# Kernel tuning notes

Hardware: AMD Instinct MI355X
Metric: run time of the kernel (lower is better)

Reference implementation:

```python
import jax, jax.numpy as jnp
from jax import lax
import numpy as np

B = 512
EPS = 1e-5


def _conv(x, w, b):
    # x: [B,C,H,W], w: [O,I,3,3], stride 1, pad 1 (same spatial)
    y = lax.conv_general_dilated(x, w, window_strides=(1, 1),
                                 padding=[(1, 1), (1, 1)],
                                 dimension_numbers=('NCHW', 'OIHW', 'NCHW'))
    return y + b[None, :, None, None]


def _bn(x, g, b, m, v):
    # eval-mode batchnorm with running stats
    inv = g * lax.rsqrt(v + EPS)
    return x * inv[None, :, None, None] + (b - m * inv)[None, :, None, None]


def _maxpool2(x):
    return lax.reduce_window(x, -jnp.inf, lax.max, (1, 1, 2, 2), (1, 1, 2, 2), 'VALID')


def _block(x, w, b, g, be, m, v):
    return _maxpool2(jax.nn.relu(_bn(_conv(x, w, b), g, be, m, v)))


def setup_inputs() -> dict:
    key = jax.random.key(0)
    ks = jax.random.split(key, 12)
    n = lambda k, s: jax.random.normal(k, s, jnp.float32) * 0.05
    z = lambda s: jnp.zeros(s, jnp.float32)
    o = lambda s: jnp.ones(s, jnp.float32)
    return {
        'x': jax.random.normal(ks[0], (B, 1, 48, 48), jnp.float32),
        'conv1_w': n(ks[1], (256, 1, 3, 3)), 'conv1_b': z((256,)),
        'bn1_g': o((256,)), 'bn1_b': z((256,)), 'bn1_m': z((256,)), 'bn1_v': o((256,)),
        'conv2_w': n(ks[2], (128, 256, 3, 3)), 'conv2_b': z((128,)),
        'bn2_g': o((128,)), 'bn2_b': z((128,)), 'bn2_m': z((128,)), 'bn2_v': o((128,)),
        'conv3_w': n(ks[3], (64, 128, 3, 3)), 'conv3_b': z((64,)),
        'bn3_g': o((64,)), 'bn3_b': z((64,)), 'bn3_m': z((64,)), 'bn3_v': o((64,)),
        'fc1_w': n(ks[4], (512, 2304)), 'fc1_b': z((512,)),
        'fc2_w': n(ks[5], (256, 512)), 'fc2_b': z((256,)),
        'att_w': n(ks[6], (64, 256)), 'att_b': z((64,)),
        'fc3_w': n(ks[7], (7, 64)), 'fc3_b': z((7,)),
    }


def reference(x, conv1_w, conv1_b, bn1_g, bn1_b, bn1_m, bn1_v,
              conv2_w, conv2_b, bn2_g, bn2_b, bn2_m, bn2_v,
              conv3_w, conv3_b, bn3_g, bn3_b, bn3_m, bn3_v,
              fc1_w, fc1_b, fc2_w, fc2_b, att_w, att_b, fc3_w, fc3_b):
    out1 = _block(x, conv1_w, conv1_b, bn1_g, bn1_b, bn1_m, bn1_v)      # [B,256,24,24]
    out2 = _block(out1, conv2_w, conv2_b, bn2_g, bn2_b, bn2_m, bn2_v)   # [B,128,12,12]
    out3 = _block(out2, conv3_w, conv3_b, bn3_g, bn3_b, bn3_m, bn3_v)   # [B,64,6,6]
    b_ = out3.shape[0]
    out4 = out3.reshape(b_, -1)                                          # [B,2304]
    out5 = out4 @ fc1_w.T + fc1_b                                        # [B,512]
    out6 = out5 @ fc2_w.T + fc2_b                                        # [B,256]
    # spatial attention: query projected to channel dim of out3
    q = out6 @ att_w.T + att_b                                           # [B,64]
    scores = jnp.einsum('bchw,bc->bhw', out3, q).reshape(b_, -1)         # [B,36]
    attn = jax.nn.softmax(scores, axis=1).reshape(b_, 6, 6)
    g_mod = jnp.einsum('bchw,bhw->bc', out3, attn)                       # [B,64]
    return g_mod @ fc3_w.T + fc3_b                                       # [B,7]
```

## Files before the change

### kernel.cpp

```cpp
#include <hip/hip_runtime.h>
#include <hip/hip_bf16.h>
#include <math.h>

#define EPS_BN 1e-5f

typedef __bf16 bf16x8 __attribute__((ext_vector_type(8)));
typedef float f32x4 __attribute__((ext_vector_type(4)));
typedef float f32x2 __attribute__((ext_vector_type(2)));

__device__ __forceinline__ void gl2lds16(const void* g, void* l) {
  __builtin_amdgcn_global_load_lds(
      (const __attribute__((address_space(1))) unsigned int*)g,
      (__attribute__((address_space(3))) unsigned int*)l, 16, 0, 0);
}

__global__ __launch_bounds__(256) void k_conv1(
    const float* __restrict__ x, const float* __restrict__ w,
    const float* __restrict__ cb, const float* __restrict__ g,
    const float* __restrict__ bb, const float* __restrict__ m,
    const float* __restrict__ v, __hip_bfloat16* __restrict__ out1p,
    __hip_bfloat16* __restrict__ out2p, const float* __restrict__ W32,
    const float* __restrict__ fc1w, float* __restrict__ Wet, int n1) {
  __shared__ float xp[14 * 50];
  const int bq = blockIdx.x;
  const int t = threadIdx.x;
  if (bq >= n1) {
    int idx = (bq - n1) * 256 + t;
    int r = idx / 2304, c = idx - r * 2304;
    float s = 0.f;
    for (int k = 0; k < 512; k++)
      s = fmaf(W32[r * 512 + k], fc1w[k * 2304 + c], s);
    Wet[c * 64 + r] = s;
    return;
  }
  const int b = bq >> 2, q = bq & 3;
  __hip_bfloat16* ob = out1p + (size_t)b * (26 * 26 * 256);
  const __hip_bfloat16 z = __float2bfloat16(0.f);
  if (q == 0)
    for (int i = t; i < 26 * 256; i += 256) ob[i] = z;
  if (q == 3)
    for (int i = t; i < 26 * 256; i += 256) ob[25 * 26 * 256 + i] = z;
  for (int i = t; i < 6 * 2 * 256; i += 256) {
    int r = 1 + 6 * q + (i >> 9), side = (i >> 8) & 1, c = i & 255;
    ob[(r * 26 + side * 25) * 256 + c] = z;
  }
  {
    __hip_bfloat16* o2 = out2p + (size_t)b * (14 * 14 * 128);
    if (q == 0)
      for (int i = t; i < 14 * 128; i += 256) o2[i] = z;
    if (q == 1)
      for (int i = t; i < 14 * 128; i += 256) o2[13 * 14 * 128 + i] = z;
    if (q == 2)
      for (int i = t; i < 6 * 2 * 128; i += 256) {
        int r = 1 + (i >> 8), side = (i >> 7) & 1, c = i & 127;
        o2[(r * 14 + side * 13) * 128 + c] = z;
      }
    if (q == 3)
      for (int i = t; i < 6 * 2 * 128; i += 256) {
        int r = 7 + (i >> 8), side = (i >> 7) & 1, c = i & 127;
        o2[(r * 14 + side * 13) * 128 + c] = z;
      }
  }
  for (int i = t; i < 14 * 50; i += 256) xp[i] = 0.f;
  __syncthreads();
  const float* xb = x + (size_t)b * 2304;
  for (int i = t; i < 14 * 48; i += 256) {
    int rr = i / 48, c = i - rr * 48;
    int gr = 12 * q - 1 + rr;
    if (gr >= 0 && gr < 48) xp[rr * 50 + c + 1] = xb[gr * 48 + c];
  }
  __syncthreads();
  float wr[9];
#pragma unroll
  for (int i = 0; i < 9; i++) wr[i] = w[t * 9 + i];
  const float scale = g[t] * rsqrtf(v[t] + EPS_BN);
  const float bias = (cb[t] - m[t]) * scale + bb[t];
#pragma unroll
  for (int ohl = 0; ohl < 6; ohl++) {
    const int r0 = 2 * ohl;
    f32x2 c01[4];
#pragma unroll
    for (int r = 0; r < 4; r++) c01[r] = *(const f32x2*)&xp[(r0 + r) * 50];
#pragma unroll 4
    for (int ow = 0; ow < 24; ow++) {
      f32x2 c23[4];
#pragma unroll
      for (int r = 0; r < 4; r++)
        c23[r] = *(const f32x2*)&xp[(r0 + r) * 50 + 2 * ow + 2];
      f32x2 s2a = 0.f, s2b = 0.f;
#pragma unroll
      for (int r = 0; r < 4; r++) {
        f32x2 p0 = c01[r], p2 = c23[r];
        f32x2 p1 = {p0.y, p2.x};
        if (r <= 2) {
          s2a += p0 * wr[r * 3 + 0];
          s2a += p1 * wr[r * 3 + 1];
          s2a += p2 * wr[r * 3 + 2];
        }
        if (r >= 1) {
          s2b += p0 * wr[(r - 1) * 3 + 0];
          s2b += p1 * wr[(r - 1) * 3 + 1];
          s2b += p2 * wr[(r - 1) * 3 + 2];
        }
      }
      f32x2 b0 = s2a * scale + bias;
      f32x2 b1 = s2b * scale + bias;
      float mx = fmaxf(fmaxf(b0.x, b0.y), fmaxf(b1.x, b1.y));
      ob[((6 * q + ohl + 1) * 26 + (ow + 1)) * 256 + t] =
          __float2bfloat16(fmaxf(mx, 0.f));
#pragma unroll
      for (int r = 0; r < 4; r++) c01[r] = c23[r];
    }
  }
}

__global__ void k_prep(const float* __restrict__ c2w,
                       __hip_bfloat16* __restrict__ wt2,
                       const float* __restrict__ c3w,
                       __hip_bfloat16* __restrict__ wt3,
                       const float* __restrict__ attw,
                       const float* __restrict__ fc2w, float* __restrict__ W32,
                       const float* __restrict__ fc1b,
                       const float* __restrict__ fc2b,
                       const float* __restrict__ attb, float* __restrict__ be) {
  const int blk = blockIdx.x, tid = threadIdx.x;
  if (blk < 1152) {
    int idx = blk * 256 + tid;
    int icr = idx & 7;
    int oc = (idx >> 3) & 127;
    int rest = idx >> 10;
    int icg = rest & 31;
    int p = rest >> 5;
    wt2[idx] = __float2bfloat16(c2w[(oc * 256 + icg * 8 + icr) * 9 + p]);
  } else if (blk < 1440) {
    int idx = (blk - 1152) * 256 + tid;
    int icr = idx & 7;
    int oc = (idx >> 3) & 63;
    int rest = idx >> 9;
    int icg = rest & 15;
    int p = rest >> 4;
    wt3[idx] = __float2bfloat16(c3w[(oc * 128 + icg * 8 + icr) * 9 + p]);
  } else if (blk < 1568) {
    int idx = (blk - 1440) * 256 + tid;
    int r = idx >> 9, c = idx & 511;
    float s = 0.f;
    for (int k = 0; k < 256; k++)
      s = fmaf(attw[r * 256 + k], fc2w[k * 512 + c], s);
    W32[idx] = s;
  } else {
    __shared__ float t1[256];
    float s = fc2b[tid];
    for (int k = 0; k < 512; k++) s = fmaf(fc2w[tid * 512 + k], fc1b[k], s);
    t1[tid] = s;
    __syncthreads();
    if (tid < 64) {
      float r = attb[tid];
      for (int k = 0; k < 256; k++) r = fmaf(attw[tid * 256 + k], t1[k], r);
      be[tid] = r;
    }
  }
}

template <int HW, int IC, int OC, int NW_M, int NW_N>
__global__ __launch_bounds__(256) void k_mconv(
    const __hip_bfloat16* __restrict__ in, const __hip_bfloat16* __restrict__ wt,
    const float* __restrict__ cb, const float* __restrict__ gg,
    const float* __restrict__ bbv, const float* __restrict__ bm,
    const float* __restrict__ bv, __hip_bfloat16* __restrict__ outp) {
  constexpr int HP = HW + 2;
  constexpr int MT = NW_M * 48;
  constexpr int ROWS = MT / HW;
  constexpr int TILES = HW / ROWS;
  constexpr int WN = OC / NW_N;
  constexpr int NF = WN / 16;
  constexpr int CP = HP;
  constexpr int NCH = 6 * CP * 8;
  constexpr int NCHP = (NCH + 255) & ~255;
  constexpr int NLD = NCHP / 256;
  constexpr int NSTG = IC / 64;
  constexpr int ABUF = NCHP * 16;
  constexpr int ICG = IC / 8;
  constexpr int EPITCH = OC + 1;
  constexpr int EBYTES = 48 * EPITCH * 4;
  constexpr int SMB = (2 * ABUF) > EBYTES ? (2 * ABUF) : EBYTES;

  __shared__ __align__(16) char smraw[SMB];
  float* se = (float*)smraw;

  const int tid = threadIdx.x;
  const int wv = tid >> 6, ln = tid & 63;
  const int wm = wv >> 1, wn = wv & 1;
  const int lhi = ln >> 4, llo = ln & 15;

  const int per = gridDim.x >> 3;
  const int xcd = blockIdx.x & 7, sl = blockIdx.x >> 3;
  const int b = xcd * (per / TILES) + sl / TILES;
  const int T = sl % TILES;
  const int h0 = T * ROWS;

  const __hip_bfloat16* inb = in + (size_t)b * HP * HP * IC;

  int srcoff[NLD];
#pragma unroll
  for (int i = 0; i < NLD; i++) {
    int ci = tid + i * 256;
    if (ci >= NCH) ci = NCH - 1;
    int kgslot = ci & 7;
    int rest = ci >> 3;
    int c = rest % CP;
    int r = rest / CP;
    int kg = kgslot ^ (c & 7);
    srcoff[i] = ((h0 + r) * HP + c) * IC + kg * 8;
  }
  int spb[3][3], msk[3][3];
#pragma unroll
  for (int mt = 0; mt < 3; mt++) {
    int m = wm * 48 + mt * 16 + llo;
    int hl = m / HW, wl = m % HW;
#pragma unroll
    for (int pw = 0; pw < 3; pw++) {
      spb[mt][pw] = (hl * CP + wl + pw) * 8;
      msk[mt][pw] = (wl + pw) & 7;
    }
  }
  const __hip_bfloat16* wtb = wt + (size_t)(lhi * OC + wn * WN + llo) * 8;

  f32x4 acc[3][NF];
  const f32x4 fz = {0.f, 0.f, 0.f, 0.f};
#pragma unroll
  for (int i = 0; i < 3; i++)
#pragma unroll
    for (int j = 0; j < NF; j++) acc[i][j] = fz;

#pragma unroll
  for (int i = 0; i < NLD; i++)
    gl2lds16(inb + srcoff[i], smraw + (tid + i * 256) * 16);
  __syncthreads();

#pragma unroll
  for (int s = 0; s < NSTG; s++) {
    if (s + 1 < NSTG) {
      char* nb = smraw + ((s + 1) & 1) * ABUF;
#pragma unroll
      for (int i = 0; i < NLD; i++)
        gl2lds16(inb + srcoff[i] + (s + 1) * 64, nb + (tid + i * 256) * 16);
    }
    const char* cw = smraw + (s & 1) * ABUF;
#pragma unroll
    for (int p = 0; p < 9; p++) {
      const int ph = p / 3, pw = p % 3;
#pragma unroll
      for (int ks = 0; ks < 2; ks++) {
        const int kg = ks * 4 + lhi;
        bf16x8 bf[NF];
#pragma unroll
        for (int j = 0; j < NF; j++)
          bf[j] = *(const bf16x8*)(wtb +
                                   ((size_t)(p * ICG + s * 8 + ks * 4) * OC) *
                                       8 +
                                   j * 128);
        bf16x8 af[3];
#pragma unroll
        for (int mt = 0; mt < 3; mt++) {
          int slot = spb[mt][pw] + ph * CP * 8 + (kg ^ msk[mt][pw]);
          af[mt] = *(const bf16x8*)(cw + slot * 16);
        }
#pragma unroll
        for (int mt = 0; mt < 3; mt++)
#pragma unroll
          for (int j = 0; j < NF; j++)
            acc[mt][j] = __builtin_amdgcn_mfma_f32_16x16x32_bf16(
                af[mt], bf[j], acc[mt][j], 0, 0, 0);
      }
    }
    __syncthreads();
  }

  constexpr int PR = 48 / HW;
  constexpr int POH = PR / 2;
  constexpr int OHW = HW / 2;
  constexpr int NP = POH * OHW * OC;
#pragma unroll
  for (int a = 0; a < NW_M; a++) {
    if (a) __syncthreads();
    if (wm == a) {
#pragma unroll
      for (int j = 0; j < NF; j++) {
        int n = wn * WN + j * 16 + llo;
        float scale = gg[n] * rsqrtf(bv[n] + EPS_BN);
        float bias = (cb[n] - bm[n]) * scale + bbv[n];
#pragma unroll
        for (int mt = 0; mt < 3; mt++)
#pragma unroll
          for (int r = 0; r < 4; r++) {
            int mrow = mt * 16 + lhi * 4 + r;
            se[mrow * EPITCH + n] = fmaxf(acc[mt][j][r] * scale + bias, 0.f);
          }
      }
    }
    __syncthreads();
    for (int s = tid; s < NP; s += 256) {
      int n = s % OC;
      int ow = (s / OC) % OHW;
      int ohl = s / (OC * OHW);
      int mloc = (2 * ohl) * HW + 2 * ow;
      float x0 = se[mloc * EPITCH + n];
      float x1 = se[(mloc + 1) * EPITCH + n];
      float x2 = se[(mloc + HW) * EPITCH + n];
      float x3 = se[(mloc + HW + 1) * EPITCH + n];
      float mx = fmaxf(fmaxf(x0, x1), fmaxf(x2, x3));
      int oh = (h0 >> 1) + a * POH + ohl;
      outp[(((size_t)b * (OHW + 2) + oh + 1) * (OHW + 2) + ow + 1) * OC + n] =
          __float2bfloat16(mx);
    }
    if (a + 1 < NW_M) __syncthreads();
  }
}

__global__ __launch_bounds__(256) void k_c3attn(
    const __hip_bfloat16* __restrict__ in, const __hip_bfloat16* __restrict__ wt,
    const float* __restrict__ cb, const float* __restrict__ gg,
    const float* __restrict__ bbv, const float* __restrict__ bm,
    const float* __restrict__ bv, const float* __restrict__ Wet,
    const float* __restrict__ be, const float* __restrict__ w3,
    const float* __restrict__ b3, float* __restrict__ out, int b0) {
  constexpr int HW = 12, IC = 128, OC = 64, HP = 14, CP = 14;
  constexpr int NCH = 14 * CP * 8;
  constexpr int NCHP = (NCH + 255) & ~255;
  constexpr int NLD = NCHP / 256;
  constexpr int NSTG = 2;
  constexpr int ABUF = NCHP * 16;
  constexpr int ICG = 16;
  constexpr int EPITCH = OC + 1;

  __shared__ __align__(16) char smraw[2 * ABUF];
  __shared__ float act[64 * 37];
  __shared__ float qp[4][64];
  __shared__ float ql[64], gm[64], sc[36];
  float* se = (float*)smraw;

  const int tid = threadIdx.x;
  const int wv = tid >> 6, ln = tid & 63;
  const int lhi = ln >> 4, llo = ln & 15;
  const int b = blockIdx.x;

  const __hip_bfloat16* inb = in + (size_t)b * HP * HP * IC;

  int srcoff[NLD];
#pragma unroll
  for (int i = 0; i < NLD; i++) {
    int ci = tid + i * 256;
    if (ci >= NCH) ci = NCH - 1;
    int kgslot = ci & 7;
    int rest = ci >> 3;
    int c = rest % CP;
    int r = rest / CP;
    int kg = kgslot ^ (c & 7);
    srcoff[i] = (r * HP + c) * IC + kg * 8;
  }
  int spb[9], wlv[9];
#pragma unroll
  for (int mt = 0; mt < 9; mt++) {
    int m = mt * 16 + llo;
    int hl = m / HW, wl = m % HW;
    spb[mt] = (hl * CP + wl) * 8;
    wlv[mt] = wl;
  }
  const __hip_bfloat16* wtb = wt + (size_t)(lhi * OC + wv * 16 + llo) * 8;

  f32x4 acc[9];
  const f32x4 fz = {0.f, 0.f, 0.f, 0.f};
#pragma unroll
  for (int i = 0; i < 9; i++) acc[i] = fz;

#pragma unroll
  for (int i = 0; i < NLD; i++)
    gl2lds16(inb + srcoff[i], smraw + (tid + i * 256) * 16);
  __syncthreads();

#pragma unroll
  for (int s = 0; s < NSTG; s++) {
    if (s + 1 < NSTG) {
      char* nb = smraw + ((s + 1) & 1) * ABUF;
#pragma unroll
      for (int i = 0; i < NLD; i++)
        gl2lds16(inb + srcoff[i] + (s + 1) * 64, nb + (tid + i * 256) * 16);
    }
    const char* cw = smraw + (s & 1) * ABUF;
#pragma unroll
    for (int tt = 0; tt < 18; tt++) {
      const int p = tt >> 1, ks = tt & 1;
      const int ph = p / 3, pw = p % 3;
      const int kg = ks * 4 + lhi;
      bf16x8 bf =
          *(const bf16x8*)(wtb + ((size_t)(p * ICG + s * 8 + ks * 4) * OC) * 8);
#pragma unroll
      for (int mt = 0; mt < 9; mt++) {
        int slot = spb[mt] + (ph * CP + pw) * 8 + (kg ^ ((wlv[mt] + pw) & 7));
        bf16x8 af = *(const bf16x8*)(cw + slot * 16);
        acc[mt] = __builtin_amdgcn_mfma_f32_16x16x32_bf16(af, bf, acc[mt], 0,
                                                          0, 0);
      }
    }
    __syncthreads();
  }

  {
    const int n = wv * 16 + llo;
    const float scale = gg[n] * rsqrtf(bv[n] + EPS_BN);
    const float bias = (cb[n] - bm[n]) * scale + bbv[n];
#pragma unroll
    for (int pz = 0; pz < 3; pz++) {
      if (pz) __syncthreads();
#pragma unroll
      for (int mtl = 0; mtl < 3; mtl++)
#pragma unroll
        for (int r = 0; r < 4; r++) {
          int mrow = mtl * 16 + lhi * 4 + r;
          se[mrow * EPITCH + n] =
              fmaxf(acc[pz * 3 + mtl][r] * scale + bias, 0.f);
        }
      __syncthreads();
      for (int sI = tid; sI < 2 * 6 * 64; sI += 256) {
        int nn = sI % 64;
        int ow = (sI / 64) % 6;
        int ohl = sI / (64 * 6);
        int mloc = (2 * ohl) * HW + 2 * ow;
        float x0 = se[mloc * EPITCH + nn];
        float x1 = se[(mloc + 1) * EPITCH + nn];
        float x2 = se[(mloc + HW) * EPITCH + nn];
        float x3 = se[(mloc + HW + 1) * EPITCH + nn];
        float mx = fmaxf(fmaxf(x0, x1), fmaxf(x2, x3));
        act[nn * 37 + (pz * 2 + ohl) * 6 + ow] = mx;
      }
    }
  }
  __syncthreads();

  {
    float qpv = 0.f;
    const int n = ln;
#pragma unroll 2
    for (int c2 = wv * 16; c2 < wv * 16 + 16; c2++)
      for (int hw = 0; hw < 36; hw++)
        qpv = fmaf(act[c2 * 37 + hw], Wet[(c2 * 36 + hw) * 64 + n], qpv);
    qp[wv][n] = qpv;
  }
  __syncthreads();
  if (tid < 64)
    ql[tid] = be[tid] + qp[0][tid] + qp[1][tid] + qp[2][tid] + qp[3][tid];
  __syncthreads();
  if (wv == 0) {
    float s = -INFINITY;
    if (ln < 36) {
      float a = 0.f;
      for (int c = 0; c < 64; c++) a = fmaf(act[c * 37 + ln], ql[c], a);
      s = a;
    }
    float mx = s;
    for (int off = 32; off >= 1; off >>= 1)
      mx = fmaxf(mx, __shfl_xor(mx, off));
    float e = (ln < 36) ? expf(s - mx) : 0.f;
    float sum = e;
    for (int off = 32; off >= 1; off >>= 1) sum += __shfl_xor(sum, off);
    if (ln < 36) sc[ln] = e / sum;
  }
  __syncthreads();
  if (wv == 0) {
    float gv = 0.f;
    for (int hw = 0; hw < 36; hw++) gv = fmaf(act[ln * 37 + hw], sc[hw], gv);
    gm[ln] = gv;
  }
  __syncthreads();
  if (tid < 7) {
    float a = b3[tid];
    for (int c = 0; c < 64; c++) a = fmaf(w3[tid * 64 + c], gm[c], a);
    out[(size_t)(b0 + b) * 7 + tid] = a;
  }
}

extern "C" void kernel_launch(void* const* d_in, const int* in_sizes, int n_in,
                              void* d_out, int out_size, void* d_ws,
                              size_t ws_size, hipStream_t stream) {
  const float* x    = (const float*)d_in[0];
  const float* c1w  = (const float*)d_in[1];
  const float* c1b  = (const float*)d_in[2];
  const float* g1   = (const float*)d_in[3];
  const float* bb1  = (const float*)d_in[4];
  const float* m1   = (const float*)d_in[5];
  const float* v1   = (const float*)d_in[6];
  const float* c2w  = (const float*)d_in[7];
  const float* c2b  = (const float*)d_in[8];
  const float* g2   = (const float*)d_in[9];
  const float* bb2  = (const float*)d_in[10];
  const float* m2   = (const float*)d_in[11];
  const float* v2   = (const float*)d_in[12];
  const float* c3w  = (const float*)d_in[13];
  const float* c3b  = (const float*)d_in[14];
  const float* g3   = (const float*)d_in[15];
  const float* bb3  = (const float*)d_in[16];
  const float* m3   = (const float*)d_in[17];
  const float* v3   = (const float*)d_in[18];
  const float* fc1w = (const float*)d_in[19];
  const float* fc1b = (const float*)d_in[20];
  const float* fc2w = (const float*)d_in[21];
  const float* fc2b = (const float*)d_in[22];
  const float* attw = (const float*)d_in[23];
  const float* attb = (const float*)d_in[24];
  const float* fc3w = (const float*)d_in[25];
  const float* fc3b = (const float*)d_in[26];

  const size_t PER_CHUNK = (173056ULL + 25088ULL) * 2;
  const size_t PERSIST = 589824 + 147456 + 131072 + 589824 + 256 + 8192;
  int CH = 512;
  while (CH > 8 && (size_t)CH * PER_CHUNK + PERSIST > ws_size) CH >>= 1;
  const int NCHK = 512 / CH;

  char* base = (char*)d_ws;
  size_t off = 0;
  auto alloc = [&](size_t nbytes) -> void* {
    void* p = base + off;
    off = (off + nbytes + 255) & ~(size_t)255;
    return p;
  };
  __hip_bfloat16* out1p = (__hip_bfloat16*)alloc((size_t)CH * 173056 * 2);
  __hip_bfloat16* out2p = (__hip_bfloat16*)alloc((size_t)CH * 25088 * 2);
  __hip_bfloat16* wt2  = (__hip_bfloat16*)alloc(589824);
  __hip_bfloat16* wt3  = (__hip_bfloat16*)alloc(147456);
  float* W32           = (float*)alloc(131072);
  float* Wet           = (float*)alloc(589824);
  float* be            = (float*)alloc(256);

  k_prep<<<1569, 256, 0, stream>>>(c2w, wt2, c3w, wt3, attw, fc2w, W32, fc1b,
                                   fc2b, attb, be);

  for (int c = 0; c < NCHK; c++) {
    const float* xc = x + (size_t)c * CH * 2304;
    const int n1 = CH * 4;
    const int grid1 = n1 + (c == 0 ? 576 : 0);
    k_conv1<<<grid1, 256, 0, stream>>>(xc, c1w, c1b, g1, bb1, m1, v1, out1p,
                                       out2p, W32, fc1w, Wet, n1);
    k_mconv<24, 256, 128, 2, 2>
        <<<CH * 6, 256, 0, stream>>>(out1p, wt2, c2b, g2, bb2, m2, v2, out2p);
    k_c3attn<<<CH, 256, 0, stream>>>(out2p, wt3, c3b, g3, bb3, m3, v3, Wet, be,
                                     fc3w, fc3b, (float*)d_out, c * CH);
  }
}
```

Baseline: 423.8 us.

## Fuse conv1, conv2 and conv3+attention into one per-image persistent kernel

```diff
diff --git a/kernel.cpp b/kernel.cpp
--- a/kernel.cpp
+++ b/kernel.cpp
@@ -12,106 +12,6 @@
   __builtin_amdgcn_global_load_lds(
       (const __attribute__((address_space(1))) unsigned int*)g,
       (__attribute__((address_space(3))) unsigned int*)l, 16, 0, 0);
-}
-
-__global__ __launch_bounds__(256) void k_conv1(
-    const float* __restrict__ x, const float* __restrict__ w,
-    const float* __restrict__ cb, const float* __restrict__ g,
-    const float* __restrict__ bb, const float* __restrict__ m,
-    const float* __restrict__ v, __hip_bfloat16* __restrict__ out1p,
-    __hip_bfloat16* __restrict__ out2p, const float* __restrict__ W32,
-    const float* __restrict__ fc1w, float* __restrict__ Wet, int n1) {
-  __shared__ float xp[14 * 50];
-  const int bq = blockIdx.x;
-  const int t = threadIdx.x;
-  if (bq >= n1) {
-    int idx = (bq - n1) * 256 + t;
-    int r = idx / 2304, c = idx - r * 2304;
-    float s = 0.f;
-    for (int k = 0; k < 512; k++)
-      s = fmaf(W32[r * 512 + k], fc1w[k * 2304 + c], s);
-    Wet[c * 64 + r] = s;
-    return;
-  }
-  const int b = bq >> 2, q = bq & 3;
-  __hip_bfloat16* ob = out1p + (size_t)b * (26 * 26 * 256);
-  const __hip_bfloat16 z = __float2bfloat16(0.f);
-  if (q == 0)
-    for (int i = t; i < 26 * 256; i += 256) ob[i] = z;
-  if (q == 3)
-    for (int i = t; i < 26 * 256; i += 256) ob[25 * 26 * 256 + i] = z;
-  for (int i = t; i < 6 * 2 * 256; i += 256) {
-    int r = 1 + 6 * q + (i >> 9), side = (i >> 8) & 1, c = i & 255;
-    ob[(r * 26 + side * 25) * 256 + c] = z;
-  }
-  {
-    __hip_bfloat16* o2 = out2p + (size_t)b * (14 * 14 * 128);
-    if (q == 0)
-      for (int i = t; i < 14 * 128; i += 256) o2[i] = z;
-    if (q == 1)
-      for (int i = t; i < 14 * 128; i += 256) o2[13 * 14 * 128 + i] = z;
-    if (q == 2)
-      for (int i = t; i < 6 * 2 * 128; i += 256) {
-        int r = 1 + (i >> 8), side = (i >> 7) & 1, c = i & 127;
-        o2[(r * 14 + side * 13) * 128 + c] = z;
-      }
-    if (q == 3)
-      for (int i = t; i < 6 * 2 * 128; i += 256) {
-        int r = 7 + (i >> 8), side = (i >> 7) & 1, c = i & 127;
-        o2[(r * 14 + side * 13) * 128 + c] = z;
-      }
-  }
-  for (int i = t; i < 14 * 50; i += 256) xp[i] = 0.f;
-  __syncthreads();
-  const float* xb = x + (size_t)b * 2304;
-  for (int i = t; i < 14 * 48; i += 256) {
-    int rr = i / 48, c = i - rr * 48;
-    int gr = 12 * q - 1 + rr;
-    if (gr >= 0 && gr < 48) xp[rr * 50 + c + 1] = xb[gr * 48 + c];
-  }
-  __syncthreads();
-  float wr[9];
-#pragma unroll
-  for (int i = 0; i < 9; i++) wr[i] = w[t * 9 + i];
-  const float scale = g[t] * rsqrtf(v[t] + EPS_BN);
-  const float bias = (cb[t] - m[t]) * scale + bb[t];
-#pragma unroll
-  for (int ohl = 0; ohl < 6; ohl++) {
-    const int r0 = 2 * ohl;
-    f32x2 c01[4];
-#pragma unroll
-    for (int r = 0; r < 4; r++) c01[r] = *(const f32x2*)&xp[(r0 + r) * 50];
-#pragma unroll 4
-    for (int ow = 0; ow < 24; ow++) {
-      f32x2 c23[4];
-#pragma unroll
-      for (int r = 0; r < 4; r++)
-        c23[r] = *(const f32x2*)&xp[(r0 + r) * 50 + 2 * ow + 2];
-      f32x2 s2a = 0.f, s2b = 0.f;
-#pragma unroll
-      for (int r = 0; r < 4; r++) {
-        f32x2 p0 = c01[r], p2 = c23[r];
-        f32x2 p1 = {p0.y, p2.x};
-        if (r <= 2) {
-          s2a += p0 * wr[r * 3 + 0];
-          s2a += p1 * wr[r * 3 + 1];
-          s2a += p2 * wr[r * 3 + 2];
-        }
-        if (r >= 1) {
-          s2b += p0 * wr[(r - 1) * 3 + 0];
-          s2b += p1 * wr[(r - 1) * 3 + 1];
-          s2b += p2 * wr[(r - 1) * 3 + 2];
-        }
-      }
-      f32x2 b0 = s2a * scale + bias;
-      f32x2 b1 = s2b * scale + bias;
-      float mx = fmaxf(fmaxf(b0.x, b0.y), fmaxf(b1.x, b1.y));
-      ob[((6 * q + ohl + 1) * 26 + (ow + 1)) * 256 + t] =
-          __float2bfloat16(fmaxf(mx, 0.f));
-#pragma unroll
-      for (int r = 0; r < 4; r++) c01[r] = c23[r];
-    }
-  }
 }
 
 __global__ void k_prep(const float* __restrict__ c2w,
@@ -161,321 +61,393 @@
   }
 }
 
-template <int HW, int IC, int OC, int NW_M, int NW_N>
-__global__ __launch_bounds__(256) void k_mconv(
-    const __hip_bfloat16* __restrict__ in, const __hip_bfloat16* __restrict__ wt,
-    const float* __restrict__ cb, const float* __restrict__ gg,
-    const float* __restrict__ bbv, const float* __restrict__ bm,
-    const float* __restrict__ bv, __hip_bfloat16* __restrict__ outp) {
-  constexpr int HP = HW + 2;
-  constexpr int MT = NW_M * 48;
-  constexpr int ROWS = MT / HW;
-  constexpr int TILES = HW / ROWS;
-  constexpr int WN = OC / NW_N;
-  constexpr int NF = WN / 16;
-  constexpr int CP = HP;
-  constexpr int NCH = 6 * CP * 8;
-  constexpr int NCHP = (NCH + 255) & ~255;
-  constexpr int NLD = NCHP / 256;
-  constexpr int NSTG = IC / 64;
-  constexpr int ABUF = NCHP * 16;
-  constexpr int ICG = IC / 8;
-  constexpr int EPITCH = OC + 1;
-  constexpr int EBYTES = 48 * EPITCH * 4;
-  constexpr int SMB = (2 * ABUF) > EBYTES ? (2 * ABUF) : EBYTES;
-
-  __shared__ __align__(16) char smraw[SMB];
-  float* se = (float*)smraw;
-
+__global__ void k_weff(const float* __restrict__ W32,
+                       const float* __restrict__ A1, float* __restrict__ Wet) {
+  int idx = blockIdx.x * 256 + threadIdx.x;
+  int r = idx / 2304, c = idx - r * 2304;
+  float s = 0.f;
+  for (int k = 0; k < 512; k++) s = fmaf(W32[r * 512 + k], A1[k * 2304 + c], s);
+  Wet[c * 64 + r] = s;
+}
+
+__global__ __launch_bounds__(256, 2) void k_pipe(
+    const float* __restrict__ x, const float* __restrict__ c1w,
+    const float* __restrict__ c1b, const float* __restrict__ g1,
+    const float* __restrict__ bb1, const float* __restrict__ m1,
+    const float* __restrict__ v1, __hip_bfloat16* __restrict__ out1p,
+    __hip_bfloat16* __restrict__ out2p, const __hip_bfloat16* __restrict__ wt2,
+    const float* __restrict__ c2b, const float* __restrict__ g2,
+    const float* __restrict__ bb2, const float* __restrict__ m2,
+    const float* __restrict__ v2, const __hip_bfloat16* __restrict__ wt3,
+    const float* __restrict__ c3b, const float* __restrict__ g3,
+    const float* __restrict__ bb3, const float* __restrict__ m3,
+    const float* __restrict__ v3, const float* __restrict__ Wet,
+    const float* __restrict__ be, const float* __restrict__ fc3w,
+    const float* __restrict__ fc3b, float* __restrict__ out, int b0) {
+  __shared__ __align__(16) char smem[44032];
+  const int blk = blockIdx.x;
   const int tid = threadIdx.x;
   const int wv = tid >> 6, ln = tid & 63;
-  const int wm = wv >> 1, wn = wv & 1;
   const int lhi = ln >> 4, llo = ln & 15;
 
-  const int per = gridDim.x >> 3;
-  const int xcd = blockIdx.x & 7, sl = blockIdx.x >> 3;
-  const int b = xcd * (per / TILES) + sl / TILES;
-  const int T = sl % TILES;
-  const int h0 = T * ROWS;
-
-  const __hip_bfloat16* inb = in + (size_t)b * HP * HP * IC;
-
-  int srcoff[NLD];
-#pragma unroll
-  for (int i = 0; i < NLD; i++) {
-    int ci = tid + i * 256;
-    if (ci >= NCH) ci = NCH - 1;
-    int kgslot = ci & 7;
-    int rest = ci >> 3;
-    int c = rest % CP;
-    int r = rest / CP;
-    int kg = kgslot ^ (c & 7);
-    srcoff[i] = ((h0 + r) * HP + c) * IC + kg * 8;
+  {
+    float* xp = (float*)smem;
+    __hip_bfloat16* ob = out1p + (size_t)blk * (26 * 26 * 256);
+    __hip_bfloat16* o2 = out2p + (size_t)blk * (14 * 14 * 128);
+    const __hip_bfloat16 z = __float2bfloat16(0.f);
+    const float* xb = x + (size_t)blk * 2304;
+    float wr[9];
+#pragma unroll
+    for (int i = 0; i < 9; i++) wr[i] = c1w[tid * 9 + i];
+    const float scale = g1[tid] * rsqrtf(v1[tid] + EPS_BN);
+    const float bias = (c1b[tid] - m1[tid]) * scale + bb1[tid];
+    for (int q = 0; q < 4; q++) {
+      __syncthreads();
+      if (q == 0)
+        for (int i = tid; i < 26 * 256; i += 256) ob[i] = z;
+      if (q == 3)
+        for (int i = tid; i < 26 * 256; i += 256) ob[25 * 26 * 256 + i] = z;
+      for (int i = tid; i < 6 * 2 * 256; i += 256) {
+        int r = 1 + 6 * q + (i >> 9), side = (i >> 8) & 1, c = i & 255;
+        ob[(r * 26 + side * 25) * 256 + c] = z;
+      }
+      if (q == 0)
+        for (int i = tid; i < 14 * 128; i += 256) o2[i] = z;
+      if (q == 1)
+        for (int i = tid; i < 14 * 128; i += 256) o2[13 * 14 * 128 + i] = z;
+      if (q == 2)
+        for (int i = tid; i < 6 * 2 * 128; i += 256) {
+          int r = 1 + (i >> 8), side = (i >> 7) & 1, c = i & 127;
+          o2[(r * 14 + side * 13) * 128 + c] = z;
+        }
+      if (q == 3)
+        for (int i = tid; i < 6 * 2 * 128; i += 256) {
+          int r = 7 + (i >> 8), side = (i >> 7) & 1, c = i & 127;
+          o2[(r * 14 + side * 13) * 128 + c] = z;
+        }
+      for (int i = tid; i < 14 * 50; i += 256) xp[i] = 0.f;
+      __syncthreads();
+      for (int i = tid; i < 14 * 48; i += 256) {
+        int rr = i / 48, c = i - rr * 48;
+        int gr = 12 * q - 1 + rr;
+        if (gr >= 0 && gr < 48) xp[rr * 50 + c + 1] = xb[gr * 48 + c];
+      }
+      __syncthreads();
+#pragma unroll
+      for (int ohl = 0; ohl < 6; ohl++) {
+        const int r0 = 2 * ohl;
+        f32x2 c01[4];
+#pragma unroll
+        for (int r = 0; r < 4; r++) c01[r] = *(const f32x2*)&xp[(r0 + r) * 50];
+#pragma unroll 4
+        for (int ow = 0; ow < 24; ow++) {
+          f32x2 c23[4];
+#pragma unroll
+          for (int r = 0; r < 4; r++)
+            c23[r] = *(const f32x2*)&xp[(r0 + r) * 50 + 2 * ow + 2];
+          f32x2 s2a = 0.f, s2b = 0.f;
+#pragma unroll
+          for (int r = 0; r < 4; r++) {
+            f32x2 p0 = c01[r], p2 = c23[r];
+            f32x2 p1 = {p0.y, p2.x};
+            if (r <= 2) {
+              s2a += p0 * wr[r * 3 + 0];
+              s2a += p1 * wr[r * 3 + 1];
+              s2a += p2 * wr[r * 3 + 2];
+            }
+            if (r >= 1) {
+              s2b += p0 * wr[(r - 1) * 3 + 0];
+              s2b += p1 * wr[(r - 1) * 3 + 1];
+              s2b += p2 * wr[(r - 1) * 3 + 2];
+            }
+          }
+          f32x2 e0 = s2a * scale + bias;
+          f32x2 e1 = s2b * scale + bias;
+          float mx = fmaxf(fmaxf(e0.x, e0.y), fmaxf(e1.x, e1.y));
+          ob[((6 * q + ohl + 1) * 26 + (ow + 1)) * 256 + tid] =
+              __float2bfloat16(fmaxf(mx, 0.f));
+#pragma unroll
+          for (int r = 0; r < 4; r++) c01[r] = c23[r];
+        }
+      }
+    }
   }
-  int spb[3][3], msk[3][3];
-#pragma unroll
-  for (int mt = 0; mt < 3; mt++) {
-    int m = wm * 48 + mt * 16 + llo;
-    int hl = m / HW, wl = m % HW;
-#pragma unroll
-    for (int pw = 0; pw < 3; pw++) {
-      spb[mt][pw] = (hl * CP + wl + pw) * 8;
-      msk[mt][pw] = (wl + pw) & 7;
-    }
-  }
-  const __hip_bfloat16* wtb = wt + (size_t)(lhi * OC + wn * WN + llo) * 8;
-
-  f32x4 acc[3][NF];
-  const f32x4 fz = {0.f, 0.f, 0.f, 0.f};
-#pragma unroll
-  for (int i = 0; i < 3; i++)
-#pragma unroll
-    for (int j = 0; j < NF; j++) acc[i][j] = fz;
-
-#pragma unroll
-  for (int i = 0; i < NLD; i++)
-    gl2lds16(inb + srcoff[i], smraw + (tid + i * 256) * 16);
-  __syncthreads();
-
-#pragma unroll
-  for (int s = 0; s < NSTG; s++) {
-    if (s + 1 < NSTG) {
-      char* nb = smraw + ((s + 1) & 1) * ABUF;
+
+  {
+    constexpr int HW = 24, IC = 256, OC = 128, HP = 26, CP = 26;
+    constexpr int NCH = 6 * CP * 8;
+    constexpr int NCHP = (NCH + 255) & ~255;
+    constexpr int NLD = NCHP / 256;
+    constexpr int NSTG = 4;
+    constexpr int ABUF = NCHP * 16;
+    constexpr int ICG = 32;
+    constexpr int EPITCH = OC + 1;
+    const int wm = wv >> 1, wn = wv & 1;
+    float* se = (float*)smem;
+
+    const __hip_bfloat16* inb = out1p + (size_t)blk * HP * HP * IC;
+    int srcoff[NLD];
+#pragma unroll
+    for (int i = 0; i < NLD; i++) {
+      int ci = tid + i * 256;
+      if (ci >= NCH) ci = NCH - 1;
+      int kgslot = ci & 7;
+      int rest = ci >> 3;
+      int c = rest % CP;
+      int r = rest / CP;
+      int kg = kgslot ^ (c & 7);
+      srcoff[i] = (r * HP + c) * IC + kg * 8;
+    }
+    int spb[3][3], msk[3][3];
+#pragma unroll
+    for (int mt = 0; mt < 3; mt++) {
+      int m = wm * 48 + mt * 16 + llo;
+      int hl = m / HW, wl = m % HW;
+#pragma unroll
+      for (int pw = 0; pw < 3; pw++) {
+        spb[mt][pw] = (hl * CP + wl + pw) * 8;
+        msk[mt][pw] = (wl + pw) & 7;
+      }
+    }
+    const __hip_bfloat16* wtb = wt2 + (size_t)(lhi * OC + wn * 64 + llo) * 8;
+
+    for (int T = 0; T < 6; T++) {
+      const int h0 = T * 4;
+      const int toff = h0 * HP * IC;
+      __syncthreads();
+      f32x4 acc[3][4];
+      const f32x4 fz = {0.f, 0.f, 0.f, 0.f};
+#pragma unroll
+      for (int i = 0; i < 3; i++)
+#pragma unroll
+        for (int j = 0; j < 4; j++) acc[i][j] = fz;
 #pragma unroll
       for (int i = 0; i < NLD; i++)
-        gl2lds16(inb + srcoff[i] + (s + 1) * 64, nb + (tid + i * 256) * 16);
-    }
-    const char* cw = smraw + (s & 1) * ABUF;
-#pragma unroll
-    for (int p = 0; p < 9; p++) {
-      const int ph = p / 3, pw = p % 3;
-#pragma unroll
-      for (int ks = 0; ks < 2; ks++) {
-        const int kg = ks * 4 + lhi;
-        bf16x8 bf[NF];
-#pragma unroll
-        for (int j = 0; j < NF; j++)
-          bf[j] = *(const bf16x8*)(wtb +
+        gl2lds16(inb + toff + srcoff[i], smem + (tid + i * 256) * 16);
+      __syncthreads();
+#pragma unroll
+      for (int s = 0; s < NSTG; s++) {
+        if (s + 1 < NSTG) {
+          char* nb = smem + ((s + 1) & 1) * ABUF;
+#pragma unroll
+          for (int i = 0; i < NLD; i++)
+            gl2lds16(inb + toff + srcoff[i] + (s + 1) * 64,
+                     nb + (tid + i * 256) * 16);
+        }
+        const char* cw = smem + (s & 1) * ABUF;
+#pragma unroll
+        for (int p = 0; p < 9; p++) {
+          const int ph = p / 3, pw = p % 3;
+#pragma unroll
+          for (int ks = 0; ks < 2; ks++) {
+            const int kg = ks * 4 + lhi;
+            bf16x8 bf[4];
+#pragma unroll
+            for (int j = 0; j < 4; j++)
+              bf[j] =
+                  *(const bf16x8*)(wtb +
                                    ((size_t)(p * ICG + s * 8 + ks * 4) * OC) *
                                        8 +
                                    j * 128);
-        bf16x8 af[3];
-#pragma unroll
-        for (int mt = 0; mt < 3; mt++) {
-          int slot = spb[mt][pw] + ph * CP * 8 + (kg ^ msk[mt][pw]);
-          af[mt] = *(const bf16x8*)(cw + slot * 16);
-        }
-#pragma unroll
-        for (int mt = 0; mt < 3; mt++)
-#pragma unroll
-          for (int j = 0; j < NF; j++)
-            acc[mt][j] = __builtin_amdgcn_mfma_f32_16x16x32_bf16(
-                af[mt], bf[j], acc[mt][j], 0, 0, 0);
-      }
-    }
-    __syncthreads();
-  }
-
-  constexpr int PR = 48 / HW;
-  constexpr int POH = PR / 2;
-  constexpr int OHW = HW / 2;
-  constexpr int NP = POH * OHW * OC;
-#pragma unroll
-  for (int a = 0; a < NW_M; a++) {
-    if (a) __syncthreads();
-    if (wm == a) {
-#pragma unroll
-      for (int j = 0; j < NF; j++) {
-        int n = wn * WN + j * 16 + llo;
-        float scale = gg[n] * rsqrtf(bv[n] + EPS_BN);
-        float bias = (cb[n] - bm[n]) * scale + bbv[n];
-#pragma unroll
-        for (int mt = 0; mt < 3; mt++)
-#pragma unroll
-          for (int r = 0; r < 4; r++) {
-            int mrow = mt * 16 + lhi * 4 + r;
-            se[mrow * EPITCH + n] = fmaxf(acc[mt][j][r] * scale + bias, 0.f);
+            bf16x8 af[3];
+#pragma unroll
+            for (int mt = 0; mt < 3; mt++) {
+              int slot = spb[mt][pw] + ph * CP * 8 + (kg ^ msk[mt][pw]);
+              af[mt] = *(const bf16x8*)(cw + slot * 16);
+            }
+#pragma unroll
+            for (int mt = 0; mt < 3; mt++)
+#pragma unroll
+              for (int j = 0; j < 4; j++)
+                acc[mt][j] = __builtin_amdgcn_mfma_f32_16x16x32_bf16(
+                    af[mt], bf[j], acc[mt][j], 0, 0, 0);
           }
-      }
-    }
-    __syncthreads();
-    for (int s = tid; s < NP; s += 256) {
-      int n = s % OC;
-      int ow = (s / OC) % OHW;
-      int ohl = s / (OC * OHW);
-      int mloc = (2 * ohl) * HW + 2 * ow;
-      float x0 = se[mloc * EPITCH + n];
-      float x1 = se[(mloc + 1) * EPITCH + n];
-      float x2 = se[(mloc + HW) * EPITCH + n];
-      float x3 = se[(mloc + HW + 1) * EPITCH + n];
-      float mx = fmaxf(fmaxf(x0, x1), fmaxf(x2, x3));
-      int oh = (h0 >> 1) + a * POH + ohl;
-      outp[(((size_t)b * (OHW + 2) + oh + 1) * (OHW + 2) + ow + 1) * OC + n] =
-          __float2bfloat16(mx);
-    }
-    if (a + 1 < NW_M) __syncthreads();
-  }
-}
-
-__global__ __launch_bounds__(256) void k_c3attn(
-    const __hip_bfloat16* __restrict__ in, const __hip_bfloat16* __restrict__ wt,
-    const float* __restrict__ cb, const float* __restrict__ gg,
-    const float* __restrict__ bbv, const float* __restrict__ bm,
-    const float* __restrict__ bv, const float* __restrict__ Wet,
-    const float* __restrict__ be, const float* __restrict__ w3,
-    const float* __restrict__ b3, float* __restrict__ out, int b0) {
-  constexpr int HW = 12, IC = 128, OC = 64, HP = 14, CP = 14;
-  constexpr int NCH = 14 * CP * 8;
-  constexpr int NCHP = (NCH + 255) & ~255;
-  constexpr int NLD = NCHP / 256;
-  constexpr int NSTG = 2;
-  constexpr int ABUF = NCHP * 16;
-  constexpr int ICG = 16;
-  constexpr int EPITCH = OC + 1;
-
-  __shared__ __align__(16) char smraw[2 * ABUF];
-  __shared__ float act[64 * 37];
-  __shared__ float qp[4][64];
-  __shared__ float ql[64], gm[64], sc[36];
-  float* se = (float*)smraw;
-
-  const int tid = threadIdx.x;
-  const int wv = tid >> 6, ln = tid & 63;
-  const int lhi = ln >> 4, llo = ln & 15;
-  const int b = blockIdx.x;
-
-  const __hip_bfloat16* inb = in + (size_t)b * HP * HP * IC;
-
-  int srcoff[NLD];
-#pragma unroll
-  for (int i = 0; i < NLD; i++) {
-    int ci = tid + i * 256;
-    if (ci >= NCH) ci = NCH - 1;
-    int kgslot = ci & 7;
-    int rest = ci >> 3;
-    int c = rest % CP;
-    int r = rest / CP;
-    int kg = kgslot ^ (c & 7);
-    srcoff[i] = (r * HP + c) * IC + kg * 8;
-  }
-  int spb[9], wlv[9];
-#pragma unroll
-  for (int mt = 0; mt < 9; mt++) {
-    int m = mt * 16 + llo;
-    int hl = m / HW, wl = m % HW;
-    spb[mt] = (hl * CP + wl) * 8;
-    wlv[mt] = wl;
-  }
-  const __hip_bfloat16* wtb = wt + (size_t)(lhi * OC + wv * 16 + llo) * 8;
-
-  f32x4 acc[9];
-  const f32x4 fz = {0.f, 0.f, 0.f, 0.f};
-#pragma unroll
-  for (int i = 0; i < 9; i++) acc[i] = fz;
-
-#pragma unroll
-  for (int i = 0; i < NLD; i++)
-    gl2lds16(inb + srcoff[i], smraw + (tid + i * 256) * 16);
-  __syncthreads();
-
-#pragma unroll
-  for (int s = 0; s < NSTG; s++) {
-    if (s + 1 < NSTG) {
-      char* nb = smraw + ((s + 1) & 1) * ABUF;
-#pragma unroll
-      for (int i = 0; i < NLD; i++)
-        gl2lds16(inb + srcoff[i] + (s + 1) * 64, nb + (tid + i * 256) * 16);
-    }
-    const char* cw = smraw + (s & 1) * ABUF;
-#pragma unroll
-    for (int tt = 0; tt < 18; tt++) {
-      const int p = tt >> 1, ks = tt & 1;
-      const int ph = p / 3, pw = p % 3;
-      const int kg = ks * 4 + lhi;
-      bf16x8 bf =
-          *(const bf16x8*)(wtb + ((size_t)(p * ICG + s * 8 + ks * 4) * OC) * 8);
-#pragma unroll
-      for (int mt = 0; mt < 9; mt++) {
-        int slot = spb[mt] + (ph * CP + pw) * 8 + (kg ^ ((wlv[mt] + pw) & 7));
-        bf16x8 af = *(const bf16x8*)(cw + slot * 16);
-        acc[mt] = __builtin_amdgcn_mfma_f32_16x16x32_bf16(af, bf, acc[mt], 0,
-                                                          0, 0);
-      }
-    }
-    __syncthreads();
-  }
-
-  {
-    const int n = wv * 16 + llo;
-    const float scale = gg[n] * rsqrtf(bv[n] + EPS_BN);
-    const float bias = (cb[n] - bm[n]) * scale + bbv[n];
-#pragma unroll
-    for (int pz = 0; pz < 3; pz++) {
-      if (pz) __syncthreads();
-#pragma unroll
-      for (int mtl = 0; mtl < 3; mtl++)
-#pragma unroll
-        for (int r = 0; r < 4; r++) {
-          int mrow = mtl * 16 + lhi * 4 + r;
-          se[mrow * EPITCH + n] =
-              fmaxf(acc[pz * 3 + mtl][r] * scale + bias, 0.f);
-        }
-      __syncthreads();
-      for (int sI = tid; sI < 2 * 6 * 64; sI += 256) {
-        int nn = sI % 64;
-        int ow = (sI / 64) % 6;
-        int ohl = sI / (64 * 6);
-        int mloc = (2 * ohl) * HW + 2 * ow;
-        float x0 = se[mloc * EPITCH + nn];
-        float x1 = se[(mloc + 1) * EPITCH + nn];
-        float x2 = se[(mloc + HW) * EPITCH + nn];
-        float x3 = se[(mloc + HW + 1) * EPITCH + nn];
-        float mx = fmaxf(fmaxf(x0, x1), fmaxf(x2, x3));
-        act[nn * 37 + (pz * 2 + ohl) * 6 + ow] = mx;
+        }
+        __syncthreads();
+      }
+      constexpr int OHW = 12;
+      constexpr int NP = 1 * OHW * OC;
+#pragma unroll
+      for (int a = 0; a < 2; a++) {
+        if (a) __syncthreads();
+        if (wm == a) {
+#pragma unroll
+          for (int j = 0; j < 4; j++) {
+            int n = wn * 64 + j * 16 + llo;
+            float scale = g2[n] * rsqrtf(v2[n] + EPS_BN);
+            float bias = (c2b[n] - m2[n]) * scale + bb2[n];
+#pragma unroll
+            for (int mt = 0; mt < 3; mt++)
+#pragma unroll
+              for (int r = 0; r < 4; r++) {
+                int mrow = mt * 16 + lhi * 4 + r;
+                se[mrow * EPITCH + n] =
+                    fmaxf(acc[mt][j][r] * scale + bias, 0.f);
+              }
+          }
+        }
+        __syncthreads();
+        for (int sI = tid; sI < NP; sI += 256) {
+          int n = sI % OC;
+          int ow = (sI / OC) % OHW;
+          int mloc = 2 * ow;
+          float x0 = se[mloc * EPITCH + n];
+          float x1 = se[(mloc + 1) * EPITCH + n];
+          float x2 = se[(mloc + HW) * EPITCH + n];
+          float x3 = se[(mloc + HW + 1) * EPITCH + n];
+          float mx = fmaxf(fmaxf(x0, x1), fmaxf(x2, x3));
+          int oh = (h0 >> 1) + a;
+          out2p[(((size_t)blk * 14 + oh + 1) * 14 + ow + 1) * OC + n] =
+              __float2bfloat16(mx);
+        }
       }
     }
   }
   __syncthreads();
 
   {
-    float qpv = 0.f;
-    const int n = ln;
+    constexpr int HW = 12, IC = 128, OC = 64, HP = 14, CP = 14;
+    constexpr int NCH = HP * CP * 4;
+    constexpr int NLD = 4;
+    constexpr int NSTG = 4;
+    constexpr int ABUF = 16384;
+    constexpr int EPITCH = OC + 1;
+    float* act = (float*)(smem + 32768);
+    float* qp = (float*)(smem + 42240);
+    float* ql = (float*)(smem + 43264);
+    float* gm = (float*)(smem + 43520);
+    float* sc = (float*)(smem + 43776);
+    float* se = (float*)smem;
+
+    const __hip_bfloat16* inb = out2p + (size_t)blk * HP * HP * IC;
+    int srcoff[NLD];
+#pragma unroll
+    for (int i = 0; i < NLD; i++) {
+      int ci = tid + i * 256;
+      if (ci >= NCH) ci = NCH - 1;
+      int kgslot = ci & 3;
+      int rest = ci >> 2;
+      int c = rest % CP;
+      int r = rest / CP;
+      int kg = kgslot ^ (c & 3);
+      srcoff[i] = (r * HP + c) * IC + kg * 8;
+    }
+    int spb[9], wlv[9];
+#pragma unroll
+    for (int mt = 0; mt < 9; mt++) {
+      int m = mt * 16 + llo;
+      int hl = m / HW, wl = m % HW;
+      spb[mt] = (hl * CP + wl) * 4;
+      wlv[mt] = wl;
+    }
+    const __hip_bfloat16* wtb = wt3 + (size_t)(lhi * OC + wv * 16 + llo) * 8;
+
+    f32x4 acc[9];
+    const f32x4 fz = {0.f, 0.f, 0.f, 0.f};
+#pragma unroll
+    for (int i = 0; i < 9; i++) acc[i] = fz;
+
+#pragma unroll
+    for (int i = 0; i < NLD; i++)
+      gl2lds16(inb + srcoff[i], smem + (tid + i * 256) * 16);
+    __syncthreads();
+#pragma unroll
+    for (int s = 0; s < NSTG; s++) {
+      if (s + 1 < NSTG) {
+        char* nb = smem + ((s + 1) & 1) * ABUF;
+#pragma unroll
+        for (int i = 0; i < NLD; i++)
+          gl2lds16(inb + srcoff[i] + (s + 1) * 32, nb + (tid + i * 256) * 16);
+      }
+      const char* cw = smem + (s & 1) * ABUF;
+#pragma unroll
+      for (int p = 0; p < 9; p++) {
+        const int ph = p / 3, pw = p % 3;
+        bf16x8 bf = *(const bf16x8*)(wtb +
+                                     ((size_t)(p * 16 + s * 4) * OC) * 8);
+#pragma unroll
+        for (int mt = 0; mt < 9; mt++) {
+          int slot =
+              spb[mt] + (ph * CP + pw) * 4 + (lhi ^ ((wlv[mt] + pw) & 3));
+          bf16x8 af = *(const bf16x8*)(cw + slot * 16);
+          acc[mt] =
+              __builtin_amdgcn_mfma_f32_16x16x32_bf16(af, bf, acc[mt], 0, 0, 0);
+        }
+      }
+      __syncthreads();
+    }
+    {
+      const int n = wv * 16 + llo;
+      const float scale = g3[n] * rsqrtf(v3[n] + EPS_BN);
+      const float bias = (c3b[n] - m3[n]) * scale + bb3[n];
+#pragma unroll
+      for (int pz = 0; pz < 3; pz++) {
+        if (pz) __syncthreads();
+#pragma unroll
+        for (int mtl = 0; mtl < 3; mtl++)
+#pragma unroll
+          for (int r = 0; r < 4; r++) {
+            int mrow = mtl * 16 + lhi * 4 + r;
+            se[mrow * EPITCH + n] =
+                fmaxf(acc[pz * 3 + mtl][r] * scale + bias, 0.f);
+          }
+        __syncthreads();
+        for (int sI = tid; sI < 2 * 6 * 64; sI += 256) {
+          int nn = sI % 64;
+          int ow = (sI / 64) % 6;
+          int ohl = sI / (64 * 6);
+          int mloc = (2 * ohl) * HW + 2 * ow;
+          float x0 = se[mloc * EPITCH + nn];
+          float x1 = se[(mloc + 1) * EPITCH + nn];
+          float x2 = se[(mloc + HW) * EPITCH + nn];
+          float x3 = se[(mloc + HW + 1) * EPITCH + nn];
+          float mx = fmaxf(fmaxf(x0, x1), fmaxf(x2, x3));
+          act[nn * 37 + (pz * 2 + ohl) * 6 + ow] = mx;
+        }
+      }
+    }
+    __syncthreads();
+    {
+      float qpv = 0.f;
+      const int n = ln;
 #pragma unroll 2
-    for (int c2 = wv * 16; c2 < wv * 16 + 16; c2++)
-      for (int hw = 0; hw < 36; hw++)
-        qpv = fmaf(act[c2 * 37 + hw], Wet[(c2 * 36 + hw) * 64 + n], qpv);
-    qp[wv][n] = qpv;
-  }
-  __syncthreads();
-  if (tid < 64)
-    ql[tid] = be[tid] + qp[0][tid] + qp[1][tid] + qp[2][tid] + qp[3][tid];
-  __syncthreads();
-  if (wv == 0) {
-    float s = -INFINITY;
-    if (ln < 36) {
-      float a = 0.f;
-      for (int c = 0; c < 64; c++) a = fmaf(act[c * 37 + ln], ql[c], a);
-      s = a;
-    }
-    float mx = s;
-    for (int off = 32; off >= 1; off >>= 1)
-      mx = fmaxf(mx, __shfl_xor(mx, off));
-    float e = (ln < 36) ? expf(s - mx) : 0.f;
-    float sum = e;
-    for (int off = 32; off >= 1; off >>= 1) sum += __shfl_xor(sum, off);
-    if (ln < 36) sc[ln] = e / sum;
-  }
-  __syncthreads();
-  if (wv == 0) {
-    float gv = 0.f;
-    for (int hw = 0; hw < 36; hw++) gv = fmaf(act[ln * 37 + hw], sc[hw], gv);
-    gm[ln] = gv;
-  }
-  __syncthreads();
-  if (tid < 7) {
-    float a = b3[tid];
-    for (int c = 0; c < 64; c++) a = fmaf(w3[tid * 64 + c], gm[c], a);
-    out[(size_t)(b0 + b) * 7 + tid] = a;
+      for (int c2 = wv * 16; c2 < wv * 16 + 16; c2++)
+        for (int hw = 0; hw < 36; hw++)
+          qpv = fmaf(act[c2 * 37 + hw], Wet[(c2 * 36 + hw) * 64 + n], qpv);
+      qp[wv * 64 + n] = qpv;
+    }
+    __syncthreads();
+    if (tid < 64)
+      ql[tid] =
+          be[tid] + qp[tid] + qp[64 + tid] + qp[128 + tid] + qp[192 + tid];
+    __syncthreads();
+    if (wv == 0) {
+      float s = -INFINITY;
+      if (ln < 36) {
+        float a = 0.f;
+        for (int c = 0; c < 64; c++) a = fmaf(act[c * 37 + ln], ql[c], a);
+        s = a;
+      }
+      float mx = s;
+      for (int off = 32; off >= 1; off >>= 1)
+        mx = fmaxf(mx, __shfl_xor(mx, off));
+      float e = (ln < 36) ? expf(s - mx) : 0.f;
+      float sum = e;
+      for (int off = 32; off >= 1; off >>= 1) sum += __shfl_xor(sum, off);
+      if (ln < 36) sc[ln] = e / sum;
+    }
+    __syncthreads();
+    if (wv == 0) {
+      float gv = 0.f;
+      for (int hw = 0; hw < 36; hw++) gv = fmaf(act[ln * 37 + hw], sc[hw], gv);
+      gm[ln] = gv;
+    }
+    __syncthreads();
+    if (tid < 7) {
+      float a = fc3b[tid];
+      for (int c = 0; c < 64; c++) a = fmaf(fc3w[tid * 64 + c], gm[c], a);
+      out[(size_t)(b0 + blk) * 7 + tid] = a;
+    }
   }
 }
 
@@ -533,16 +505,13 @@
 
   k_prep<<<1569, 256, 0, stream>>>(c2w, wt2, c3w, wt3, attw, fc2w, W32, fc1b,
                                    fc2b, attb, be);
+  k_weff<<<576, 256, 0, stream>>>(W32, fc1w, Wet);
 
   for (int c = 0; c < NCHK; c++) {
     const float* xc = x + (size_t)c * CH * 2304;
-    const int n1 = CH * 4;
-    const int grid1 = n1 + (c == 0 ? 576 : 0);
-    k_conv1<<<grid1, 256, 0, stream>>>(xc, c1w, c1b, g1, bb1, m1, v1, out1p,
-                                       out2p, W32, fc1w, Wet, n1);
-    k_mconv<24, 256, 128, 2, 2>
-        <<<CH * 6, 256, 0, stream>>>(out1p, wt2, c2b, g2, bb2, m2, v2, out2p);
-    k_c3attn<<<CH, 256, 0, stream>>>(out2p, wt3, c3b, g3, bb3, m3, v3, Wet, be,
-                                     fc3w, fc3b, (float*)d_out, c * CH);
+    k_pipe<<<CH, 256, 0, stream>>>(xc, c1w, c1b, g1, bb1, m1, v1, out1p, out2p,
+                                   wt2, c2b, g2, bb2, m2, v2, wt3, c3b, g3,
+                                   bb3, m3, v3, Wet, be, fc3w, fc3b,
+                                   (float*)d_out, c * CH);
   }
 }
```

Measured after the change: 1.264 ms. 198% more time.
